# Kernel tuning notes

Hardware: AMD Instinct MI355X
Metric: run time of the kernel (lower is better)

Reference implementation:

```python
import jax, jax.numpy as jnp
import numpy as np

N, D = 2097152, 10  # tokens, feature dim (pinned by nn.Linear(10,10))


def setup_inputs() -> dict:
    key = jax.random.key(0)
    kx, kr, kw1, kb1, kw2, kb2 = jax.random.split(key, 6)
    s = 1.0 / np.sqrt(D)  # torch nn.Linear default init range
    x = jax.random.normal(kx, (N, D), dtype=jnp.float32)
    route = jax.random.randint(kr, (N,), 0, 2, dtype=jnp.int32)  # RandScatter decision
    W1 = jax.random.uniform(kw1, (D, D), jnp.float32, -s, s)
    b1 = jax.random.uniform(kb1, (D,), jnp.float32, -s, s)
    W2 = jax.random.uniform(kw2, (D, D), jnp.float32, -s, s)
    b2 = jax.random.uniform(kb2, (D,), jnp.float32, -s, s)
    return {"x": x, "W1": W1, "b1": b1, "W2": W2, "b2": b2, "route": route}


def reference(x, W1, b1, W2, b2, route):
    # Original: scatter rows by `route` to expert1/expert2 (Linear 10->10),
    # then gather back to original row order. Equivalent dense form:
    # out[i] = expert_{route[i]}(x[i]). The 10x10 GEMMs are negligible, so
    # computing both branches and selecting is the efficient vectorized form.
    y0 = x @ W1.T + b1  # [N, D] expert1 on all rows
    y1 = x @ W2.T + b2  # [N, D] expert2 on all rows
    return jnp.where((route == 0)[:, None], y0, y1)
```

## Files before the change

kernel.cpp:

```cpp
#include <hip/hip_runtime.h>


#define BLOCK 256
#define D 10
#define WAVE_ROWS 128
#define F4_PER_WAVE 320
#define ROWS_PER_BLOCK 512

typedef float f4 __attribute__((ext_vector_type(4)));
typedef float f2 __attribute__((ext_vector_type(2)));

__global__ __launch_bounds__(BLOCK) void moe_kernel(
    const float* __restrict__ x,
    const float* __restrict__ W1,
    const float* __restrict__ b1,
    const float* __restrict__ W2,
    const float* __restrict__ b2,
    const int*   __restrict__ route,
    float*       __restrict__ out,
    int n)
{
    __shared__ f4 lds[(BLOCK / 64) * F4_PER_WAVE];

    const int lane = threadIdx.x & 63;
    const int wave = threadIdx.x >> 6;
    f4* __restrict__ wlds = lds + wave * F4_PER_WAVE;

    const long long rowbase =
        ((long long)blockIdx.x * (BLOCK / 64) + wave) * WAVE_ROWS;

    if (rowbase + WAVE_ROWS <= n) {
        const f4* __restrict__ xv = (const f4*)(x + rowbase * D);
        const int2 rt = ((const int2*)(route + rowbase))[lane];

        float xf[2 * D];
        #pragma unroll
        for (int j = 0; j < 5; ++j) {
            f4 t = xv[lane * 5 + j];
            xf[4 * j + 0] = t.x; xf[4 * j + 1] = t.y;
            xf[4 * j + 2] = t.z; xf[4 * j + 3] = t.w;
        }

        f2 xp[D];
        #pragma unroll
        for (int k = 0; k < D; ++k)
            xp[k] = (f2){xf[k], xf[D + k]};

        float o0[D], o1[D];
        #pragma unroll
        for (int j = 0; j < D; ++j) {
            f2 a0 = (f2){b1[j], b1[j]};
            f2 a1 = (f2){b2[j], b2[j]};
            #pragma unroll
            for (int k = 0; k < D; ++k) {
                const float w1 = W1[j * D + k];
                const float w2 = W2[j * D + k];
                a0 = __builtin_elementwise_fma(xp[k], (f2){w1, w1}, a0);
                a1 = __builtin_elementwise_fma(xp[k], (f2){w2, w2}, a1);
            }
            o0[j] = rt.x ? a1.x : a0.x;
            o1[j] = rt.y ? a1.y : a0.y;
        }

        {
            f4 t0 = (f4){o0[0], o0[1], o0[2], o0[3]};
            f4 t1 = (f4){o0[4], o0[5], o0[6], o0[7]};
            f4 t2 = (f4){o0[8], o0[9], o1[0], o1[1]};
            f4 t3 = (f4){o1[2], o1[3], o1[4], o1[5]};
            f4 t4 = (f4){o1[6], o1[7], o1[8], o1[9]};
            wlds[lane * 5 + 0] = t0;
            wlds[lane * 5 + 1] = t1;
            wlds[lane * 5 + 2] = t2;
            wlds[lane * 5 + 3] = t3;
            wlds[lane * 5 + 4] = t4;
        }
        __builtin_amdgcn_wave_barrier();

        f4* __restrict__ ov = (f4*)(out + rowbase * D);
        #pragma unroll
        for (int j = 0; j < 5; ++j)
            ov[j * 64 + lane] = wlds[j * 64 + lane];
    } else {
        for (int r = 0; r < 2; ++r) {
            const long long row = rowbase + lane * 2 + r;
            if (row < n) {
                const int sel = route[row];
                for (int j = 0; j < D; ++j) {
                    float y0 = b1[j];
                    float y1 = b2[j];
                    for (int k = 0; k < D; ++k) {
                        const float xk = x[row * D + k];
                        y0 = fmaf(xk, W1[j * D + k], y0);
                        y1 = fmaf(xk, W2[j * D + k], y1);
                    }
                    out[row * D + j] = sel ? y1 : y0;
                }
            }
        }
    }
}

extern "C" void kernel_launch(void* const* d_in, const int* in_sizes, int n_in,
                              void* d_out, int out_size, void* d_ws, size_t ws_size,
                              hipStream_t stream) {
    const float* x     = (const float*)d_in[0];
    const float* W1    = (const float*)d_in[1];
    const float* b1    = (const float*)d_in[2];
    const float* W2    = (const float*)d_in[3];
    const float* b2    = (const float*)d_in[4];
    const int*   route = (const int*)d_in[5];
    float*       out   = (float*)d_out;

    const int n = in_sizes[5];
    const int blocks = (n + ROWS_PER_BLOCK - 1) / ROWS_PER_BLOCK;

    moe_kernel<<<blocks, BLOCK, 0, stream>>>(x, W1, b1, W2, b2, route, out, n);
}
```

Before: 164.2 us.

## Use grid-stride persistent blocks and store outputs directly without LDS staging

The launch grid is capped at 2048 blocks, and each block loops over 512-row chunks in a grid-stride pattern. This cuts block launch overhead and lets the weight loads be reused across iterations. The LDS transpose staging is also removed, so each lane writes its five f4 outputs to strided addresses. That makes the global stores less coalesced: a wave's store instruction now touches addresses 80 bytes apart instead of a contiguous span. The diff also leaves a dead variable computation behind.

```diff
diff --git a/kernel.cpp b/kernel.cpp
--- a/kernel.cpp
+++ b/kernel.cpp
@@ -4,8 +4,8 @@
 #define BLOCK 256
 #define D 10
 #define WAVE_ROWS 128
-#define F4_PER_WAVE 320
-#define ROWS_PER_BLOCK 512
+#define CHUNK_ROWS 512
+#define GRID_BLOCKS 2048
 
 typedef float f4 __attribute__((ext_vector_type(4)));
 typedef float f2 __attribute__((ext_vector_type(2)));
@@ -20,80 +20,80 @@
     float*       __restrict__ out,
     int n)
 {
-    __shared__ f4 lds[(BLOCK / 64) * F4_PER_WAVE];
-
     const int lane = threadIdx.x & 63;
     const int wave = threadIdx.x >> 6;
-    f4* __restrict__ wlds = lds + wave * F4_PER_WAVE;
 
-    const long long rowbase =
-        ((long long)blockIdx.x * (BLOCK / 64) + wave) * WAVE_ROWS;
+    const int nchunks = (n + CHUNK_ROWS - 1) / CHUNK_ROWS;
 
-    if (rowbase + WAVE_ROWS <= n) {
-        const f4* __restrict__ xv = (const f4*)(x + rowbase * D);
-        const int2 rt = ((const int2*)(route + rowbase))[lane];
+    for (int c = blockIdx.x; c < nchunks; c += gridDim.x) {
+        const long long rowbase =
+            (long long)c * CHUNK_ROWS + wave * WAVE_ROWS;
 
-        float xf[2 * D];
-        #pragma unroll
-        for (int j = 0; j < 5; ++j) {
-            f4 t = xv[lane * 5 + j];
-            xf[4 * j + 0] = t.x; xf[4 * j + 1] = t.y;
-            xf[4 * j + 2] = t.z; xf[4 * j + 3] = t.w;
-        }
+        if (rowbase + WAVE_ROWS <= n) {
+            const f4* __restrict__ xv = (const f4*)(x + rowbase * D);
+            const int2 rt = ((const int2*)(route + rowbase))[lane];
 
-        f2 xp[D];
-        #pragma unroll
-        for (int k = 0; k < D; ++k)
-            xp[k] = (f2){xf[k], xf[D + k]};
+            float xf[2 * D];
+            #pragma unroll
+            for (int j = 0; j < 5; ++j) {
+                f4 t = xv[lane * 5 + j];
+                xf[4 * j + 0] = t.x; xf[4 * j + 1] = t.y;
+                xf[4 * j + 2] = t.z; xf[4 * j + 3] = t.w;
+            }
 
-        float o0[D], o1[D];
-        #pragma unroll
-        for (int j = 0; j < D; ++j) {
-            f2 a0 = (f2){b1[j], b1[j]};
-            f2 a1 = (f2){b2[j], b2[j]};
+            f2 xp[D];
             #pragma unroll
-            for (int k = 0; k < D; ++k) {
-                const float w1 = W1[j * D + k];
-                const float w2 = W2[j * D + k];
-                a0 = __builtin_elementwise_fma(xp[k], (f2){w1, w1}, a0);
-                a1 = __builtin_elementwise_fma(xp[k], (f2){w2, w2}, a1);
+            for (int k = 0; k < D; ++k)
+                xp[k] = (f2){xf[k], xf[D + k]};
+
+            float o0[D], o1[D];
+            #pragma unroll
+            for (int j = 0; j < D; ++j) {
+                f2 a0 = (f2){b1[j], b1[j]};
+                f2 a1 = (f2){b2[j], b2[j]};
+                #pragma unroll
+                for (int k = 0; k < D; ++k) {
+                    const float w1 = W1[j * D + k];
+                    const float w2 = W2[j * D + k];
+                    a0 = __builtin_elementwise_fma(xp[k], (f2){w1, w1}, a0);
+                    a1 = __builtin_elementwise_fma(xp[k], (f2){w2, w2}, a1);
+                }
+                o0[j] = rt.x ? a1.x : a0.x;
+                o1[j] = rt.y ? a1.y : a0.y;
             }
-            o0[j] = rt.x ? a1.x : a0.x;
-            o1[j] = rt.y ? a1.y : a0.y;
-        }
 
-        {
-            f4 t0 = (f4){o0[0], o0[1], o0[2], o0[3]};
-            f4 t1 = (f4){o0[4], o0[5], o0[6], o0[7]};
-            f4 t2 = (f4){o0[8], o0[9], o1[0], o1[1]};
-            f4 t3 = (f4){o1[2], o1[3], o1[4], o1[5]};
-            f4 t4 = (f4){o1[6], o1[7], o1[8], o1[9]};
-            wlds[lane * 5 + 0] = t0;
-            wlds[lane * 5 + 1] = t1;
-            wlds[lane * 5 + 2] = t2;
-            wlds[lane * 5 + 3] = t3;
-            wlds[lane * 5 + 4] = t4;
-        }
-        __builtin_amdgcn_wave_barrier();
-
-        f4* __restrict__ ov = (f4*)(out + rowbase * D);
-        #pragma unroll
-        for (int j = 0; j < 5; ++j)
-            ov[j * 64 + lane] = wlds[j * 64 + lane];
-    } else {
-        for (int r = 0; r < 2; ++r) {
-            const long long row = rowbase + lane * 2 + r;
-            if (row < n) {
-                const int sel = route[row];
-                for (int j = 0; j < D; ++j) {
-                    float y0 = b1[j];
-                    float y1 = b2[j];
-                    for (int k = 0; k < D; ++k) {
-                        const float xk = x[row * D + k];
-                        y0 = fmaf(xk, W1[j * D + k], y0);
-                        y1 = fmaf(xk, W2[j * D + k], y1);
+            f4* __restrict__ ov = (f4*)(out + rowbase * D);
+            #pragma unroll
+            for (int j = 0; j < 5; ++j) {
+                f4 t;
+                t.x = (j < 2) ? o0[4 * j + 0]
+                    : (j == 2 ? o0[8] : o1[4 * (j - 3) + 2]);
+                (void)t;
+                f4 s;
+                switch (j) {
+                    case 0: s = (f4){o0[0], o0[1], o0[2], o0[3]}; break;
+                    case 1: s = (f4){o0[4], o0[5], o0[6], o0[7]}; break;
+                    case 2: s = (f4){o0[8], o0[9], o1[0], o1[1]}; break;
+                    case 3: s = (f4){o1[2], o1[3], o1[4], o1[5]}; break;
+                    default: s = (f4){o1[6], o1[7], o1[8], o1[9]}; break;
+                }
+                ov[lane * 5 + j] = s;
+            }
+        } else {
+            for (int r = 0; r < 2; ++r) {
+                const long long row = rowbase + lane * 2 + r;
+                if (row < n) {
+                    const int sel = route[row];
+                    for (int j = 0; j < D; ++j) {
+                        float y0 = b1[j];
+                        float y1 = b2[j];
+                        for (int k = 0; k < D; ++k) {
+                            const float xk = x[row * D + k];
+                            y0 = fmaf(xk, W1[j * D + k], y0);
+                            y1 = fmaf(xk, W2[j * D + k], y1);
+                        }
+                        out[row * D + j] = sel ? y1 : y0;
                     }
-                    out[row * D + j] = sel ? y1 : y0;
                 }
             }
         }
@@ -112,7 +112,8 @@
     float*       out   = (float*)d_out;
 
     const int n = in_sizes[5];
-    const int blocks = (n + ROWS_PER_BLOCK - 1) / ROWS_PER_BLOCK;
+    const int nchunks = (n + CHUNK_ROWS - 1) / CHUNK_ROWS;
+    const int blocks = nchunks < GRID_BLOCKS ? nchunks : GRID_BLOCKS;
 
     moe_kernel<<<blocks, BLOCK, 0, stream>>>(x, W1, b1, W2, b2, route, out, n);
 }
```

New measurement: 167.5 us. No clear change (+2.0%).
